# Kernel tuning notes

Measured on AMD Instinct MI355X. Metric: run time of the kernel, lower is better.

Reference implementation:

```python
import jax, jax.numpy as jnp
import numpy as np
from jax import lax

B_, L_, D_MODEL = 2, 2048, 1024
H, P, N, G, K, CHUNK = 32, 64, 128, 1, 4, 256
INTER = H * P                 # 2048
CONV_DIM = INTER + 2 * G * N  # 2304
PROJ = INTER + CONV_DIM + H   # 4384: [gate | hidden_B_C | dt]
EPS = 1e-6


def segment_sum(x):
    # x: [..., T] -> [..., T, T]; segsum[i,j] = sum_{k=j+1..i} x[k] for i>=j, else -inf
    T = x.shape[-1]
    xx = jnp.repeat(x[..., None], T, axis=-1)
    xx = jnp.where(jnp.tril(jnp.ones((T, T), bool), -1), xx, 0.0)
    s = jnp.cumsum(xx, axis=-2)
    return jnp.where(jnp.tril(jnp.ones((T, T), bool)), s, -jnp.inf)


def setup_inputs() -> dict:
    key = jax.random.key(0)
    ks = jax.random.split(key, 6)
    s = 0.02
    return {
        "x": jax.random.normal(ks[0], (B_, L_, D_MODEL), jnp.float32),
        "in_proj_w": jax.random.normal(ks[1], (PROJ, D_MODEL), jnp.float32) * s,
        "conv_w": jax.random.normal(ks[2], (CONV_DIM, 1, K), jnp.float32) * s,
        "conv_b": jnp.zeros((CONV_DIM,), jnp.float32),
        "dt_bias": jax.random.uniform(ks[3], (H,), jnp.float32, 0.0, 1.0),
        "A_log": jnp.log(jnp.arange(1, H + 1, dtype=jnp.float32)),
        "D": jnp.ones((H,), jnp.float32),
        "norm_w": jnp.ones((INTER,), jnp.float32),
        "out_proj_w": jax.random.normal(ks[4], (D_MODEL, INTER), jnp.float32) * s,
    }


def _forward(x, in_proj_w, conv_w, conv_b, dt_bias, A_log, D, norm_w, out_proj_w):
    b, L, _ = x.shape
    proj = x @ in_proj_w.T                                    # [b,L,PROJ]
    gate, hBC, dt = jnp.split(proj, [INTER, INTER + CONV_DIM], axis=-1)
    # depthwise causal conv1d over sequence
    xc = jnp.pad(hBC.transpose(0, 2, 1), ((0, 0), (0, 0), (K - 1, 0)))
    conv = lax.conv_general_dilated(xc, conv_w, (1,), 'VALID',
                                    dimension_numbers=('NCH', 'OIH', 'NCH'),
                                    feature_group_count=CONV_DIM)
    hBC = jax.nn.silu((conv + conv_b[None, :, None]).transpose(0, 2, 1))  # [b,L,CONV_DIM]
    hs, Bm, Cm = jnp.split(hBC, [INTER, INTER + G * N], axis=-1)
    hs = hs.reshape(b, L, H, P)
    Bm = jnp.repeat(Bm.reshape(b, L, G, N), H // G, axis=2)   # [b,L,H,N]
    Cm = jnp.repeat(Cm.reshape(b, L, G, N), H // G, axis=2)
    dt = jax.nn.softplus(dt + dt_bias)                        # [b,L,H]
    A = -jnp.exp(A_log)                                       # [H]
    D_res = hs * D[None, None, :, None]
    hs = hs * dt[..., None]
    Adt = dt * A                                              # [b,L,H]
    c = L // CHUNK
    A_c = Adt.reshape(b, c, CHUNK, H).transpose(0, 3, 1, 2)   # [b,H,c,l]
    A_cum = jnp.cumsum(A_c, axis=-1)
    Lmat = jnp.exp(segment_sum(A_c))                          # [b,H,c,l,l]
    hs_c = hs.reshape(b, c, CHUNK, H, P)
    B_c = Bm.reshape(b, c, CHUNK, H, N)
    C_c = Cm.reshape(b, c, CHUNK, H, N)
    # intra-chunk (diagonal blocks)
    Gm = jnp.einsum('bcshn,bczhn->bchsz', C_c, B_c)
    M = Gm * Lmat.transpose(0, 2, 1, 3, 4)
    Y_diag = jnp.einsum('bchsz,bczhp->bcshp', M, hs_c)
    # per-chunk final states
    decay_states = jnp.exp(A_cum[..., -1:] - A_cum)           # [b,H,c,l]
    B_decay = B_c * decay_states.transpose(0, 2, 3, 1)[..., None]
    states = jnp.einsum('bclhn,bclhp->bchpn', B_decay, hs_c)  # [b,c,H,P,N]
    # inter-chunk recurrence
    decay_chunk = jnp.exp(segment_sum(jnp.pad(A_cum[..., -1], ((0, 0), (0, 0), (1, 0)))))  # [b,H,c+1,c+1]
    states0 = jnp.concatenate([jnp.zeros_like(states[:, :1]), states], axis=1)             # [b,c+1,H,P,N]
    prev = jnp.einsum('bhij,bjhpn->bihpn', decay_chunk, states0)[:, :-1]                   # [b,c,H,P,N]
    # off-diagonal contribution
    state_decay = jnp.exp(A_cum).transpose(0, 2, 3, 1)        # [b,c,l,H]
    Y_off = jnp.einsum('bclhn,bchpn->bclhp', C_c, prev) * state_decay[..., None]
    y = ((Y_diag + Y_off).reshape(b, L, H, P) + D_res).reshape(b, L, INTER)
    # gated grouped RMSNorm (group_size = INTER // G)
    gs = INTER // G
    yf = y.astype(jnp.float32) * jax.nn.silu(gate.astype(jnp.float32))
    yg = yf.reshape(b, L, INTER // gs, gs)
    var = jnp.mean(yg * yg, axis=-1, keepdims=True)
    yn = (yg * lax.rsqrt(var + EPS)).reshape(b, L, INTER) * norm_w
    return yn @ out_proj_w.T


def reference(x, in_proj_w, conv_w, conv_b, dt_bias, A_log, D, norm_w, out_proj_w):
    return _forward(x, in_proj_w, conv_w, conv_b, dt_bias, A_log, D, norm_w, out_proj_w)
```

## Files before the change

kernel.cpp:

```cpp
#include <hip/hip_runtime.h>
#include <stdint.h>

typedef __attribute__((ext_vector_type(8))) short short8;
typedef __attribute__((ext_vector_type(4))) float f32x4;

#define DEV static __device__ __forceinline__

DEV float b2f(unsigned short u) { union { float f; unsigned int i; } x; x.i = ((unsigned int)u) << 16; return x.f; }
DEV unsigned short f2b(float f) {
    union { float f; unsigned int i; } x; x.f = f;
    unsigned int r = x.i + 0x7fffu + ((x.i >> 16) & 1u);
    return (unsigned short)(r >> 16);
}
DEV void gld_lds16(const void* g, void* l) {
    __builtin_amdgcn_global_load_lds((const __attribute__((address_space(1))) void*)g,
                                     (__attribute__((address_space(3))) void*)l, 16, 0, 0);
}
DEV int xcd_swizzle(int bid, int nwg) {
    int q = nwg >> 3, r = nwg & 7;
    int xcd = bid & 7, base = bid >> 3;
    return (xcd < r ? xcd * (q + 1) : r * (q + 1) + (xcd - r) * q) + base;
}

__global__ void cast_f32_to_bf16(const float* __restrict__ in, unsigned short* __restrict__ out, long n8) {
    long i = (long)blockIdx.x * blockDim.x + threadIdx.x;
    long stride = (long)gridDim.x * blockDim.x;
    for (; i < n8; i += stride) {
        const f32x4* p = (const f32x4*)(in + i * 8);
        f32x4 a = p[0], b = p[1];
        short8 o;
        o[0] = (short)f2b(a[0]); o[1] = (short)f2b(a[1]); o[2] = (short)f2b(a[2]); o[3] = (short)f2b(a[3]);
        o[4] = (short)f2b(b[0]); o[5] = (short)f2b(b[1]); o[6] = (short)f2b(b[2]); o[7] = (short)f2b(b[3]);
        *(short8*)(out + i * 8) = o;
    }
}

template<int OMODE>
__global__ __launch_bounds__(256) void gemm_nt(
    const unsigned short* __restrict__ A, int lda, long sAy, long sAz,
    const unsigned short* __restrict__ B, int ldb, long sBy, long sBz,
    void* __restrict__ Cp, int ldc, long sCy, long sCz,
    float* __restrict__ dtout,
    int M, int N, int K, int tn)
{
    A += (long)blockIdx.y * sAy + (long)blockIdx.z * sAz;
    B += (long)blockIdx.y * sBy + (long)blockIdx.z * sBz;
    int bid = xcd_swizzle(blockIdx.x, gridDim.x);
    int im = bid / tn, in_ = bid % tn;
    int m0 = im * 128, n0 = in_ * 128;
    __shared__ short smem[2 * 128 * 64];
    short* As = smem;
    short* Bs = smem + 128 * 64;
    int tid = threadIdx.x;
    int lane = tid & 63, wave = tid >> 6;
    int wu = __builtin_amdgcn_readfirstlane(wave);
    int wm = wave >> 1, wn = wave & 1;
    f32x4 acc[4][4];
#pragma unroll
    for (int m = 0; m < 4; m++)
#pragma unroll
        for (int n = 0; n < 4; n++) acc[m][n] = (f32x4){0.f, 0.f, 0.f, 0.f};

    for (int k0 = 0; k0 < K; k0 += 64) {
#pragma unroll
        for (int i = 0; i < 4; ++i) {
            int g = i * 256 + tid;
            int r = g >> 3, pc = g & 7;
            int cc = pc ^ (r & 7);
            const unsigned short* srcA = A + (long)(m0 + r) * lda + k0 + cc * 8;
            gld_lds16(srcA, As + (i * 256 + wu * 64) * 8);
            int rb = n0 + r; rb = rb < N ? rb : N - 1;
            const unsigned short* srcB = B + (long)rb * ldb + k0 + cc * 8;
            gld_lds16(srcB, Bs + (i * 256 + wu * 64) * 8);
        }
        __syncthreads();
#pragma unroll
        for (int ks = 0; ks < 2; ++ks) {
            short8 af[4], bfr[4];
#pragma unroll
            for (int m = 0; m < 4; ++m) {
                int r = wm * 64 + m * 16 + (lane & 15);
                int pc = (ks * 4 + (lane >> 4)) ^ (r & 7);
                af[m] = *(const short8*)(As + r * 64 + pc * 8);
            }
#pragma unroll
            for (int n = 0; n < 4; ++n) {
                int r = wn * 64 + n * 16 + (lane & 15);
                int pc = (ks * 4 + (lane >> 4)) ^ (r & 7);
                bfr[n] = *(const short8*)(Bs + r * 64 + pc * 8);
            }
#pragma unroll
            for (int m = 0; m < 4; ++m)
#pragma unroll
                for (int n = 0; n < 4; ++n)
                    acc[m][n] = __builtin_amdgcn_mfma_f32_16x16x32_bf16(af[m], bfr[n], acc[m][n], 0, 0, 0);
        }
        __syncthreads();
    }
    int rbase = m0 + wm * 64 + ((lane >> 4) << 2);
    int cbase = n0 + wn * 64 + (lane & 15);
    if (OMODE == 0) {
        float* C = (float*)Cp;
        C += (long)blockIdx.y * sCy + (long)blockIdx.z * sCz;
#pragma unroll
        for (int m = 0; m < 4; ++m)
#pragma unroll
            for (int n = 0; n < 4; ++n) {
                int col = cbase + n * 16;
                if (col < N) {
#pragma unroll
                    for (int r = 0; r < 4; ++r)
                        C[(long)(rbase + m * 16 + r) * ldc + col] = acc[m][n][r];
                }
            }
    } else {
        if (OMODE == 2) {
#pragma unroll
            for (int m = 0; m < 4; ++m)
#pragma unroll
                for (int n = 0; n < 4; ++n) {
                    int col = cbase + n * 16;
                    if (col >= 4352 && col < N) {
#pragma unroll
                        for (int r = 0; r < 4; ++r)
                            dtout[(long)(rbase + m * 16 + r) * 32 + (col - 4352)] = acc[m][n][r];
                    }
                }
        }
        unsigned short* Cs = (unsigned short*)smem;
        int rl = wm * 64 + ((lane >> 4) << 2);
        int cl = wn * 64 + (lane & 15);
#pragma unroll
        for (int m = 0; m < 4; ++m)
#pragma unroll
            for (int r = 0; r < 4; ++r) {
                int row = rl + m * 16 + r;
                int xr = ((row >> 2) & 3) << 4;
#pragma unroll
                for (int n = 0; n < 4; ++n)
                    Cs[row * 128 + ((cl + n * 16) ^ xr)] = f2b(acc[m][n][r]);
            }
        __syncthreads();
        unsigned short* C = (unsigned short*)Cp;
        C += (long)blockIdx.y * sCy + (long)blockIdx.z * sCz;
#pragma unroll
        for (int j = 0; j < 8; ++j) {
            int chunk = j * 256 + tid;
            int row = chunk >> 4, c8 = (chunk & 15) * 8;
            int col = n0 + c8;
            int xr = ((row >> 2) & 3) << 4;
            bool ok = (col < N) && !(OMODE == 2 && col >= 4352);
            if (ok)
                *(short8*)(C + (long)(m0 + row) * ldc + col) = *(const short8*)(Cs + row * 128 + (c8 ^ xr));
        }
    }
}

__global__ __launch_bounds__(256) void conv_dt_kernel(
    const unsigned short* __restrict__ projb,
    const float* __restrict__ dtraw,
    const float* __restrict__ conv_w, const float* __restrict__ conv_b,
    const float* __restrict__ dt_bias, const float* __restrict__ A_log,
    unsigned short* __restrict__ hs, unsigned short* __restrict__ Bb, unsigned short* __restrict__ Cb,
    float* __restrict__ dtv, float* __restrict__ dtA)
{
    int row = blockIdx.x;
    int b = row >> 11, t = row & 2047;
    int tid = threadIdx.x;
    if (tid < 32) {
        float v = dtraw[(long)row * 32 + tid] + dt_bias[tid];
        float dt = v > 20.f ? v : log1pf(__expf(v));
        dtv[(long)(b * 32 + tid) * 2048 + t] = dt;
        dtA[(long)(b * 32 + tid) * 2048 + t] = -dt * __expf(A_log[tid]);
    }
    int ch0 = tid * 8;
    float a[8];
    {
        const f32x4* cb = (const f32x4*)(conv_b + ch0);
        f32x4 b0 = cb[0], b1 = cb[1];
#pragma unroll
        for (int j = 0; j < 4; ++j) { a[j] = b0[j]; a[4 + j] = b1[j]; }
    }
    f32x4 wv[8];
#pragma unroll
    for (int j = 0; j < 8; ++j) wv[j] = *(const f32x4*)(conv_w + (ch0 + j) * 4);
#pragma unroll
    for (int k = 0; k < 4; ++k) {
        int tt = t - 3 + k;
        if (tt >= 0) {
            short8 v = *(const short8*)(projb + (long)(b * 2048 + tt) * 4384 + 2048 + ch0);
#pragma unroll
            for (int j = 0; j < 8; ++j) a[j] += b2f((unsigned short)v[j]) * wv[j][k];
        }
    }
    short8 o;
#pragma unroll
    for (int j = 0; j < 8; ++j) { float s = a[j] / (1.f + __expf(-a[j])); o[j] = (short)f2b(s); }
    *(short8*)(hs + (long)row * 2048 + ch0) = o;
    {
        int ch = 2048 + tid;
        float acc2 = conv_b[ch];
#pragma unroll
        for (int k = 0; k < 4; ++k) {
            int tt = t - 3 + k;
            if (tt >= 0) acc2 += b2f(projb[(long)(b * 2048 + tt) * 4384 + 2048 + ch]) * conv_w[ch * 4 + k];
        }
        float s = acc2 / (1.f + __expf(-acc2));
        if (tid < 128) Bb[(long)row * 128 + tid] = f2b(s);
        else           Cb[(long)row * 128 + tid - 128] = f2b(s);
    }
}

__global__ __launch_bounds__(256) void cumsum_kernel(
    const float* __restrict__ dtA, float* __restrict__ Acum, float* __restrict__ Atot)
{
    int blk = blockIdx.x;
    int c = blk & 7, bh = blk >> 3;
    int l = threadIdx.x;
    __shared__ float s[256];
    float v = dtA[(long)bh * 2048 + c * 256 + l];
    s[l] = v;
    __syncthreads();
    for (int off = 1; off < 256; off <<= 1) {
        float x = (l >= off) ? s[l - off] : 0.f;
        __syncthreads();
        s[l] += x;
        __syncthreads();
    }
    Acum[(long)bh * 2048 + c * 256 + l] = s[l];
    if (l == 255) Atot[bh * 8 + c] = s[255];
}

__global__ __launch_bounds__(256) void transpose_kernel(
    const unsigned short* __restrict__ hs,
    const unsigned short* __restrict__ Bb,
    const float* __restrict__ dtv,
    const float* __restrict__ Acum,
    const float* __restrict__ Atot,
    unsigned short* __restrict__ xdtT,
    unsigned short* __restrict__ xdtd,
    unsigned short* __restrict__ BT)
{
    int b = blockIdx.y;
    int ct = blockIdx.x >> 5;
    int tt = blockIdx.x & 31;
    int c0 = ct * 64, t0 = tt * 64;
    __shared__ float tile[64][65];
    int tid = threadIdx.x;
    bool isB = (c0 >= 2048);
#pragma unroll
    for (int i = 0; i < 2; ++i) {
        int ci = i * 256 + tid;
        int r = ci >> 3, c8 = (ci & 7) * 8;
        const unsigned short* src;
        if (!isB) src = hs + ((long)(b * 2048 + t0 + r)) * 2048 + c0 + c8;
        else      src = Bb + ((long)(b * 2048 + t0 + r)) * 128 + (c0 - 2048) + c8;
        short8 v = *(const short8*)src;
#pragma unroll
        for (int j = 0; j < 8; ++j) tile[r][c8 + j] = b2f((unsigned short)v[j]);
    }
    __syncthreads();
#pragma unroll
    for (int i = 0; i < 2; ++i) {
        int co = i * 256 + tid;
        int oc = co >> 3, tc8 = (co & 7) * 8;
        int ch = c0 + oc;
        if (!isB) {
            int h = ch >> 6;
            long bh = b * 32 + h;
            short8 o1, o2;
#pragma unroll
            for (int j = 0; j < 8; ++j) {
                int t = t0 + tc8 + j;
                float v = tile[tc8 + j][oc];
                float dt = dtv[bh * 2048 + t];
                float dec = __expf(Atot[bh * 8 + (t >> 8)] - Acum[bh * 2048 + t]);
                float xv = v * dt;
                o1[j] = (short)f2b(xv);
                o2[j] = (short)f2b(xv * dec);
            }
            long off = ((long)(b * 2048 + ch)) * 2048 + t0 + tc8;
            *(short8*)(xdtT + off) = o1;
            *(short8*)(xdtd + off) = o2;
        } else {
            short8 o;
#pragma unroll
            for (int j = 0; j < 8; ++j) o[j] = (short)f2b(tile[tc8 + j][oc]);
            long off = ((long)(b * 128 + (ch - 2048))) * 2048 + t0 + tc8;
            *(short8*)(BT + off) = o;
        }
    }
}

__global__ __launch_bounds__(256) void ydiagoff_kernel(
    const unsigned short* __restrict__ Gm,
    const float* __restrict__ Acum,
    const unsigned short* __restrict__ xdtT,
    const unsigned short* __restrict__ hs,
    const unsigned short* __restrict__ Cb,
    const unsigned short* __restrict__ prevb,
    const float* __restrict__ Dp,
    float* __restrict__ y)
{
    int blk = blockIdx.x;
    int h = blk & 31, bc = blk >> 5;
    int c = bc & 7, b = bc >> 3;
    int tid = threadIdx.x, lane = tid & 63, wave = tid >> 6;
    __shared__ float sAc[256];
    __shared__ short Mb[256 * 64];
    sAc[tid] = Acum[(long)(b * 32 + h) * 2048 + c * 256 + tid];
    __syncthreads();
    f32x4 acc[4][4];
#pragma unroll
    for (int m = 0; m < 4; m++)
#pragma unroll
        for (int n = 0; n < 4; n++) acc[m][n] = (f32x4){0.f, 0.f, 0.f, 0.f};

    for (int zp = 0; zp < 4; ++zp) {
#pragma unroll
        for (int i = 0; i < 8; ++i) {
            int ci = i * 256 + tid;
            int s = ci >> 3, cz = ci & 7;
            int z0 = zp * 64 + cz * 8;
            short8 gv = *(const short8*)(Gm + ((long)bc * 256 + s) * 256 + z0);
            float as = sAc[s];
            short8 o;
#pragma unroll
            for (int j = 0; j < 8; ++j) {
                int z = z0 + j;
                float e = (s >= z) ? __expf(as - sAc[z]) : 0.f;
                o[j] = (short)f2b(b2f((unsigned short)gv[j]) * e);
            }
            *(short8*)(Mb + s * 64 + (cz ^ (s & 7)) * 8) = o;
        }
        __syncthreads();
#pragma unroll
        for (int ks = 0; ks < 2; ++ks) {
            short8 af[4], bfr[4];
#pragma unroll
            for (int m = 0; m < 4; ++m) {
                int r = wave * 64 + m * 16 + (lane & 15);
                int pc = (ks * 4 + (lane >> 4)) ^ (r & 7);
                af[m] = *(const short8*)(Mb + r * 64 + pc * 8);
            }
#pragma unroll
            for (int n = 0; n < 4; ++n) {
                int p = n * 16 + (lane & 15);
                int z = c * 256 + zp * 64 + ks * 32 + (lane >> 4) * 8;
                bfr[n] = *(const short8*)(xdtT + ((long)(b * 2048) + h * 64 + p) * 2048 + z);
            }
#pragma unroll
            for (int m = 0; m < 4; ++m)
#pragma unroll
                for (int n = 0; n < 4; ++n)
                    acc[m][n] = __builtin_amdgcn_mfma_f32_16x16x32_bf16(af[m], bfr[n], acc[m][n], 0, 0, 0);
        }
        __syncthreads();
    }
    float el[4];
#pragma unroll
    for (int m = 0; m < 4; ++m) el[m] = __expf(sAc[wave * 64 + m * 16 + (lane & 15)]);
#pragma unroll
    for (int ks = 0; ks < 4; ++ks) {
        short8 af[4], bfr[4];
#pragma unroll
        for (int m = 0; m < 4; ++m) {
            int l = wave * 64 + m * 16 + (lane & 15);
            short8 cv = *(const short8*)(Cb + ((long)b * 2048 + c * 256 + l) * 128 + ks * 32 + (lane >> 4) * 8);
#pragma unroll
            for (int j = 0; j < 8; ++j) af[m][j] = (short)f2b(b2f((unsigned short)cv[j]) * el[m]);
        }
#pragma unroll
        for (int n = 0; n < 4; ++n) {
            int p = n * 16 + (lane & 15);
            bfr[n] = *(const short8*)(prevb + ((long)(bc * 32 + h) * 64 + p) * 128 + ks * 32 + (lane >> 4) * 8);
        }
#pragma unroll
        for (int m = 0; m < 4; ++m)
#pragma unroll
            for (int n = 0; n < 4; ++n)
                acc[m][n] = __builtin_amdgcn_mfma_f32_16x16x32_bf16(af[m], bfr[n], acc[m][n], 0, 0, 0);
    }
    float Dv = Dp[h];
#pragma unroll
    for (int m = 0; m < 4; ++m)
#pragma unroll
        for (int n = 0; n < 4; ++n) {
            int p = n * 16 + (lane & 15);
            int ch = h * 64 + p;
#pragma unroll
            for (int r = 0; r < 4; ++r) {
                int s = wave * 64 + m * 16 + ((lane >> 4) << 2) + r;
                long row_g = (long)b * 2048 + c * 256 + s;
                y[row_g * 2048 + ch] = acc[m][n][r] + b2f(hs[row_g * 2048 + ch]) * Dv;
            }
        }
}

__global__ __launch_bounds__(256) void scan_kernel(
    const float* __restrict__ states,
    const float* __restrict__ Atot,
    unsigned short* __restrict__ prevb)
{
    int bh = blockIdx.x;
    int b = bh >> 5, h = bh & 31;
    float ex[8];
#pragma unroll
    for (int c = 0; c < 8; ++c) ex[c] = __expf(Atot[bh * 8 + c]);
    for (int e = threadIdx.x; e < 8192; e += 256) {
        float S = 0.f;
#pragma unroll
        for (int c = 0; c < 8; ++c) {
            long idx = (long)((b * 8 + c) * 32 + h) * 8192 + e;
            prevb[idx] = f2b(S);
            S = ex[c] * S + states[idx];
        }
    }
}

__global__ __launch_bounds__(256) void rmsnorm_kernel(
    const float* __restrict__ y, const unsigned short* __restrict__ projb,
    const float* __restrict__ norm_w, unsigned short* __restrict__ yn)
{
    int row = blockIdx.x;
    int tid = threadIdx.x, lane = tid & 63, wave = tid >> 6;
    int ch0 = tid * 8;
    const f32x4* yp = (const f32x4*)(y + (long)row * 2048 + ch0);
    f32x4 yv0 = yp[0], yv1 = yp[1];
    short8 g8 = *(const short8*)(projb + (long)row * 4384 + ch0);
    float v[8];
    float ss = 0.f;
#pragma unroll
    for (int j = 0; j < 8; ++j) {
        float g = b2f((unsigned short)g8[j]);
        float s = g / (1.f + __expf(-g));
        float yv = (j < 4) ? yv0[j] : yv1[j - 4];
        v[j] = yv * s; ss += v[j] * v[j];
    }
#pragma unroll
    for (int off = 1; off < 64; off <<= 1) ss += __shfl_xor(ss, off);
    __shared__ float sw[4];
    if (lane == 0) sw[wave] = ss;
    __syncthreads();
    float tot = sw[0] + sw[1] + sw[2] + sw[3];
    float scale = rsqrtf(tot * (1.f / 2048.f) + 1e-6f);
    short8 o;
#pragma unroll
    for (int j = 0; j < 8; ++j) o[j] = (short)f2b(v[j] * scale * norm_w[ch0 + j]);
    *(short8*)(yn + (long)row * 2048 + ch0) = o;
}

extern "C" void kernel_launch(void* const* d_in, const int* in_sizes, int n_in,
                              void* d_out, int out_size, void* d_ws, size_t ws_size,
                              hipStream_t stream)
{
    const float* x        = (const float*)d_in[0];
    const float* in_proj  = (const float*)d_in[1];
    const float* conv_w   = (const float*)d_in[2];
    const float* conv_b   = (const float*)d_in[3];
    const float* dt_bias  = (const float*)d_in[4];
    const float* A_log    = (const float*)d_in[5];
    const float* Dp       = (const float*)d_in[6];
    const float* norm_w   = (const float*)d_in[7];
    const float* out_proj = (const float*)d_in[8];
    float* out = (float*)d_out;

    char* w = (char*)d_ws;
    auto alloc = [&](size_t bytes) { char* p = w; w += (bytes + 255) & ~(size_t)255; return p; };
    unsigned short* xb    = (unsigned short*)alloc(4096L * 1024 * 2);
    unsigned short* wb    = (unsigned short*)alloc(4384L * 1024 * 2);
    unsigned short* ob    = (unsigned short*)alloc(1024L * 2048 * 2);
    unsigned short* projb = (unsigned short*)alloc(4096L * 4384 * 2);
    float*          dtraw = (float*)        alloc(4096L * 32 * 4);
    unsigned short* hs    = (unsigned short*)alloc(4096L * 2048 * 2);
    unsigned short* Bb    = (unsigned short*)alloc(4096L * 128 * 2);
    unsigned short* Cb    = (unsigned short*)alloc(4096L * 128 * 2);
    float*          dtv   = (float*)        alloc(64L * 2048 * 4);
    float*          dtA   = (float*)        alloc(64L * 2048 * 4);
    float*          Acum  = (float*)        alloc(64L * 2048 * 4);
    float*          Atot  = (float*)        alloc(64L * 8 * 4);
    unsigned short* xdtT  = (unsigned short*)alloc(2L * 2048 * 2048 * 2);
    unsigned short* xdtd  = (unsigned short*)alloc(2L * 2048 * 2048 * 2);
    unsigned short* BT    = (unsigned short*)alloc(2L * 128 * 2048 * 2);
    unsigned short* Gmb   = (unsigned short*)alloc(16L * 256 * 256 * 2);
    float*          yb    = (float*)        alloc(4096L * 2048 * 4);
    float*          states= (float*)        alloc(2L * 8 * 2048 * 128 * 4);
    unsigned short* prevb = (unsigned short*)alloc(2L * 8 * 2048 * 128 * 2);
    unsigned short* yn    = (unsigned short*)alloc(4096L * 2048 * 2);

    cast_f32_to_bf16<<<2048, 256, 0, stream>>>(x, xb, 4096L * 1024 / 8);
    cast_f32_to_bf16<<<2048, 256, 0, stream>>>(in_proj, wb, 4384L * 1024 / 8);
    cast_f32_to_bf16<<<1024, 256, 0, stream>>>(out_proj, ob, 1024L * 2048 / 8);

    gemm_nt<2><<<dim3(32 * 35, 1, 1), 256, 0, stream>>>(
        xb, 1024, 0, 0, wb, 1024, 0, 0, projb, 4384, 0, 0, dtraw, 4096, 4384, 1024, 35);

    conv_dt_kernel<<<4096, 256, 0, stream>>>(projb, dtraw, conv_w, conv_b, dt_bias, A_log,
                                             hs, Bb, Cb, dtv, dtA);

    cumsum_kernel<<<512, 256, 0, stream>>>(dtA, Acum, Atot);

    transpose_kernel<<<dim3(34 * 32, 2, 1), 256, 0, stream>>>(hs, Bb, dtv, Acum, Atot, xdtT, xdtd, BT);

    gemm_nt<1><<<dim3(4, 8, 2), 256, 0, stream>>>(
        Cb, 128, 256L * 128, 2048L * 128,
        Bb, 128, 256L * 128, 2048L * 128,
        Gmb, 256, 256L * 256, 8L * 256 * 256, nullptr, 256, 256, 128, 2);

    gemm_nt<0><<<dim3(16, 8, 2), 256, 0, stream>>>(
        xdtd, 2048, 256, 2048L * 2048,
        BT, 2048, 256, 128L * 2048,
        states, 128, 2048L * 128, 8L * 2048 * 128, nullptr, 2048, 128, 256, 1);

    scan_kernel<<<64, 256, 0, stream>>>(states, Atot, prevb);

    ydiagoff_kernel<<<512, 256, 0, stream>>>(Gmb, Acum, xdtT, hs, Cb, prevb, Dp, yb);

    rmsnorm_kernel<<<4096, 256, 0, stream>>>(yb, projb, norm_w, yn);

    gemm_nt<0><<<dim3(32 * 8, 1, 1), 256, 0, stream>>>(
        yn, 2048, 0, 0, ob, 2048, 0, 0, out, 1024, 0, 0, nullptr, 4096, 1024, 2048, 8);
}
```

Before: 327.4 us.

## Double-buffer GEMM LDS tiles with async prefetch and merge cast kernels

The shared GEMM kernel now uses two LDS stages, so the next K-tile's global-to-LDS loads are issued before computing on the current tile, with explicit vmcnt waits and raw barriers replacing __syncthreads. MFMA sections are wrapped in s_setprio to favour math issue. The three fp32-to-bf16 cast launches are merged into one kernel to cut launch overhead. Doubling LDS to 64KB per block may reduce occupancy, and the hand-written waitcnt depends on the exact count of outstanding loads.

```diff
diff --git a/kernel.cpp b/kernel.cpp
--- a/kernel.cpp
+++ b/kernel.cpp
@@ -22,16 +22,23 @@
     return (xcd < r ? xcd * (q + 1) : r * (q + 1) + (xcd - r) * q) + base;
 }
 
-__global__ void cast_f32_to_bf16(const float* __restrict__ in, unsigned short* __restrict__ out, long n8) {
+__global__ void cast3_kernel(const float* __restrict__ a, unsigned short* __restrict__ oa, long na8,
+                             const float* __restrict__ b, unsigned short* __restrict__ ob_, long nb8,
+                             const float* __restrict__ c, unsigned short* __restrict__ oc, long nc8) {
     long i = (long)blockIdx.x * blockDim.x + threadIdx.x;
     long stride = (long)gridDim.x * blockDim.x;
-    for (; i < n8; i += stride) {
-        const f32x4* p = (const f32x4*)(in + i * 8);
-        f32x4 a = p[0], b = p[1];
+    long tot = na8 + nb8 + nc8;
+    for (; i < tot; i += stride) {
+        const float* src; unsigned short* dst; long j = i;
+        if (j < na8) { src = a; dst = oa; }
+        else if (j < na8 + nb8) { j -= na8; src = b; dst = ob_; }
+        else { j -= na8 + nb8; src = c; dst = oc; }
+        const f32x4* p = (const f32x4*)(src + j * 8);
+        f32x4 v0 = p[0], v1 = p[1];
         short8 o;
-        o[0] = (short)f2b(a[0]); o[1] = (short)f2b(a[1]); o[2] = (short)f2b(a[2]); o[3] = (short)f2b(a[3]);
-        o[4] = (short)f2b(b[0]); o[5] = (short)f2b(b[1]); o[6] = (short)f2b(b[2]); o[7] = (short)f2b(b[3]);
-        *(short8*)(out + i * 8) = o;
+        o[0] = (short)f2b(v0[0]); o[1] = (short)f2b(v0[1]); o[2] = (short)f2b(v0[2]); o[3] = (short)f2b(v0[3]);
+        o[4] = (short)f2b(v1[0]); o[5] = (short)f2b(v1[1]); o[6] = (short)f2b(v1[2]); o[7] = (short)f2b(v1[3]);
+        *(short8*)(dst + j * 8) = o;
     }
 }
 
@@ -48,9 +55,7 @@
     int bid = xcd_swizzle(blockIdx.x, gridDim.x);
     int im = bid / tn, in_ = bid % tn;
     int m0 = im * 128, n0 = in_ * 128;
-    __shared__ short smem[2 * 128 * 64];
-    short* As = smem;
-    short* Bs = smem + 128 * 64;
+    __shared__ short smem[2 * 2 * 128 * 64];
     int tid = threadIdx.x;
     int lane = tid & 63, wave = tid >> 6;
     int wu = __builtin_amdgcn_readfirstlane(wave);
@@ -61,19 +66,33 @@
 #pragma unroll
         for (int n = 0; n < 4; n++) acc[m][n] = (f32x4){0.f, 0.f, 0.f, 0.f};
 
-    for (int k0 = 0; k0 < K; k0 += 64) {
+    auto stage = [&](int k0, int s) {
+        short* As = smem + s * 16384;
+        short* Bs = As + 8192;
 #pragma unroll
         for (int i = 0; i < 4; ++i) {
             int g = i * 256 + tid;
             int r = g >> 3, pc = g & 7;
             int cc = pc ^ (r & 7);
-            const unsigned short* srcA = A + (long)(m0 + r) * lda + k0 + cc * 8;
-            gld_lds16(srcA, As + (i * 256 + wu * 64) * 8);
+            gld_lds16(A + (long)(m0 + r) * lda + k0 + cc * 8, As + (i * 256 + wu * 64) * 8);
             int rb = n0 + r; rb = rb < N ? rb : N - 1;
-            const unsigned short* srcB = B + (long)rb * ldb + k0 + cc * 8;
-            gld_lds16(srcB, Bs + (i * 256 + wu * 64) * 8);
-        }
-        __syncthreads();
+            gld_lds16(B + (long)rb * ldb + k0 + cc * 8, Bs + (i * 256 + wu * 64) * 8);
+        }
+    };
+
+    int nt = K >> 6;
+    stage(0, 0);
+    for (int t = 0; t < nt; ++t) {
+        int cur = t & 1;
+        if (t + 1 < nt) {
+            stage((t + 1) << 6, cur ^ 1);
+            asm volatile("s_waitcnt vmcnt(8)" ::: "memory");
+        } else {
+            asm volatile("s_waitcnt vmcnt(0)" ::: "memory");
+        }
+        __builtin_amdgcn_s_barrier();
+        const short* As = smem + cur * 16384;
+        const short* Bs = As + 8192;
 #pragma unroll
         for (int ks = 0; ks < 2; ++ks) {
             short8 af[4], bfr[4];
@@ -89,14 +108,17 @@
                 int pc = (ks * 4 + (lane >> 4)) ^ (r & 7);
                 bfr[n] = *(const short8*)(Bs + r * 64 + pc * 8);
             }
+            __builtin_amdgcn_s_setprio(1);
 #pragma unroll
             for (int m = 0; m < 4; ++m)
 #pragma unroll
                 for (int n = 0; n < 4; ++n)
                     acc[m][n] = __builtin_amdgcn_mfma_f32_16x16x32_bf16(af[m], bfr[n], acc[m][n], 0, 0, 0);
-        }
-        __syncthreads();
-    }
+            __builtin_amdgcn_s_setprio(0);
+        }
+        __builtin_amdgcn_s_barrier();
+    }
+
     int rbase = m0 + wm * 64 + ((lane >> 4) << 2);
     int cbase = n0 + wn * 64 + (lane & 15);
     if (OMODE == 0) {
@@ -488,9 +510,9 @@
     unsigned short* prevb = (unsigned short*)alloc(2L * 8 * 2048 * 128 * 2);
     unsigned short* yn    = (unsigned short*)alloc(4096L * 2048 * 2);
 
-    cast_f32_to_bf16<<<2048, 256, 0, stream>>>(x, xb, 4096L * 1024 / 8);
-    cast_f32_to_bf16<<<2048, 256, 0, stream>>>(in_proj, wb, 4384L * 1024 / 8);
-    cast_f32_to_bf16<<<1024, 256, 0, stream>>>(out_proj, ob, 1024L * 2048 / 8);
+    cast3_kernel<<<2048, 256, 0, stream>>>(x, xb, 4096L * 1024 / 8,
+                                           in_proj, wb, 4384L * 1024 / 8,
+                                           out_proj, ob, 1024L * 2048 / 8);
 
     gemm_nt<2><<<dim3(32 * 35, 1, 1), 256, 0, stream>>>(
         xb, 1024, 0, 0, wb, 1024, 0, 0, projb, 4384, 0, 0, dtraw, 4096, 4384, 1024, 35);
```

Result: faster. 299.1 us (-8.6%).
